# Kernel tuning notes

Hardware: AMD Instinct MI355X
Metric: run time of the kernel (lower is better)

## Reference

```python
import jax, jax.numpy as jnp
import numpy as np

E = 100000   # num entities
D = 300      # embedding dim
R = 1000     # num relations
T = 10000    # aligned pairs
K = 25       # negatives per pair
GAMMA = 1.0


def spmm(rows, cols, vals, x, n_rows):
    # sparse(COO) @ dense: out[r] = sum_{nnz: rows==r} vals * x[cols]
    return jax.ops.segment_sum(vals[:, None] * x[cols], rows, num_segments=n_rows)


def setup_inputs() -> dict:
    key = jax.random.key(0)
    ks = jax.random.split(key, 24)
    g = lambda i, s: jax.random.normal(ks[i], s, dtype=jnp.float32) * 0.05
    ri = lambda i, s, hi: jax.random.randint(ks[i], s, 0, hi, dtype=jnp.int32)
    ru = lambda i, s: jax.random.uniform(ks[i], s, dtype=jnp.float32)
    return {
        'word_embedding': jax.random.normal(ks[0], (E, D), dtype=jnp.float32),
        'kernel_gate': g(1, (D, D)),
        'bias_gate': jnp.zeros((D,), jnp.float32),
        'W1': g(2, (D, D)),
        'W2': g(3, (D, D)),
        'Dense': g(4, (3 * D, D)),
        'Bias': jnp.zeros((D,), jnp.float32),
        'hr_rows': ri(5, (300000,), R), 'hr_cols': ri(6, (300000,), E), 'hr_vals': ru(7, (300000,)),
        'tr_rows': ri(8, (300000,), R), 'tr_cols': ri(9, (300000,), E), 'tr_vals': ru(10, (300000,)),
        'er_rows': ri(11, (300000,), E), 'er_cols': ri(12, (300000,), 2 * R), 'er_vals': ru(13, (300000,)),
        'adj_rows': ri(14, (600000,), E), 'adj_cols': ri(15, (600000,), E), 'adj_vals': ru(16, (600000,)),
        'pos_left': ri(17, (T,), E), 'pos_right': ri(18, (T,), E),
        'neg_right': ri(19, (T, K), E), 'neg_left': ri(20, (T, K), E),
        'mask': jnp.ones((T, K), jnp.float32),
    }


def highway(layer1, layer2, kernel_gate, bias_gate):
    tg = jax.nn.sigmoid(layer1 @ kernel_gate + bias_gate)
    return tg * layer2 + (1.0 - tg) * layer1


def reference(word_embedding, kernel_gate, bias_gate, W1, W2, Dense, Bias,
              hr_rows, hr_cols, hr_vals, tr_rows, tr_cols, tr_vals,
              er_rows, er_cols, er_vals, adj_rows, adj_cols, adj_vals,
              pos_left, pos_right, neg_right, neg_left, mask):
    # L2-normalized frozen word embeddings
    emb = word_embedding / jnp.linalg.norm(word_embedding, axis=-1, keepdims=True)

    # Global relation aggregation (compute_r)
    L = spmm(hr_rows, hr_cols, hr_vals, emb, R)          # [R, D]
    Rm = spmm(tr_rows, tr_cols, tr_vals, emb, R)         # [R, D]
    r_fwd = jnp.concatenate([L, Rm], axis=-1)            # [R, 2D]
    r_emb = jnp.concatenate([r_fwd, -r_fwd], axis=0)     # [2R, 2D]
    nb = spmm(er_rows, er_cols, er_vals, r_emb, E)       # [E, 2D]
    h = jnp.concatenate([emb, nb], axis=-1)              # [E, 3D]
    h = emb + jax.nn.relu(h @ Dense + Bias)

    # Local relation aggregation: 2-layer highway GCN
    gcn1 = jax.nn.relu(spmm(adj_rows, adj_cols, adj_vals, h @ W1, E))
    hg1 = highway(h, gcn1, kernel_gate, bias_gate)
    gcn2 = jax.nn.relu(spmm(adj_rows, adj_cols, adj_vals, hg1 @ W2, E))
    node = highway(hg1, gcn2, kernel_gate, bias_gate)    # [E, D]

    # Hinge alignment loss
    l_x = node[pos_left]                                 # [T, D]
    r_x = node[pos_right]                                # [T, D]
    Dm = jnp.sum(jnp.abs(l_x - r_x), axis=1) + GAMMA     # [T]
    B1 = jnp.sum(jnp.abs(l_x[:, None, :] - node[neg_right]), axis=-1)  # [T, K]
    L1 = jax.nn.relu(Dm[:, None] - B1) * mask
    B2 = jnp.sum(jnp.abs(node[neg_left] - r_x[:, None, :]), axis=-1)   # [T, K]
    L2 = jax.nn.relu(Dm[:, None] - B2) * mask
    return (jnp.sum(L1) + jnp.sum(L2)) / 2.0
```

## Files before the change

### kernel.cpp

```cpp
#include <hip/hip_runtime.h>
#include <math.h>

#define E_N 100000
#define D_N 300
#define R_N 1000
#define T_N 10000
#define K_N 25
#define DP  320
#define BM  64
#define NT  1563

typedef __attribute__((ext_vector_type(8))) short bf16x8;
typedef __attribute__((ext_vector_type(4))) float f32x4;

__device__ __forceinline__ float bf2f(unsigned short h){
  union{ unsigned int u; float f; } c; c.u = ((unsigned int)h)<<16; return c.f;
}
__device__ __forceinline__ unsigned short f2bf(float f){
  union{ float f; unsigned int u; } c; c.f = f;
  unsigned int u = c.u + 0x7FFFu + ((c.u>>16)&1u);
  return (unsigned short)(u>>16);
}
__device__ __forceinline__ unsigned int pack2(float lo, float hi){
  return ((unsigned int)f2bf(hi)<<16) | f2bf(lo);
}

static constexpr size_t BUFB   = (size_t)100032*DP*2;
static constexpr size_t BUFU8  = (size_t)100032*DP;
static constexpr size_t OFF_B0    = 0;
static constexpr size_t OFF_B1    = BUFB;
static constexpr size_t OFF_B2    = 2*BUFB;
static constexpr size_t OFF_B3    = 3*BUFB;
static constexpr size_t OFF_RFWD  = OFF_B3 + BUFU8;
static constexpr size_t OFF_G     = OFF_RFWD + 1310720;
static constexpr size_t OFF_WTKG  = OFF_RFWD + 2400000;
static constexpr size_t OFF_WTW1  = OFF_WTKG + 204800;
static constexpr size_t OFF_WTW2  = OFF_WTW1 + 204800;
static constexpr size_t OFF_WTDN  = OFF_WTW2 + 204800;
static constexpr size_t OFF_WTDN2 = OFF_WTDN + 204800;
static constexpr size_t OFF_BIASP = OFF_WTDN2 + 409600;
static constexpr size_t OFF_BGP   = OFF_BIASP + 1280;
static constexpr size_t OFF_PTRHR = OFF_BGP + 1280;
static constexpr size_t OFF_PTRTR = OFF_PTRHR + 4096;
static constexpr size_t OFF_PTRER = OFF_PTRTR + 4096;
static constexpr size_t OFF_PTRADJ= OFF_PTRER + 400896;
static constexpr size_t OFF_CURHR = OFF_PTRADJ + 400896;
static constexpr size_t OFF_CURTR = OFF_CURHR + 4096;
static constexpr size_t OFF_CURER = OFF_CURTR + 4096;
static constexpr size_t OFF_CURADJ= OFF_CURER + 400896;
static constexpr size_t SZ_CURALL = 4096+4096+400896+400896;
static constexpr size_t OFF_SPHR  = OFF_CURADJ + 400896;
static constexpr size_t OFF_SPTR  = OFF_SPHR + 2400000;
static constexpr size_t OFF_SPER  = OFF_SPTR + 2400000;
static constexpr size_t OFF_SPAD  = OFF_SPER + 2400000;
static constexpr size_t OFF_PART  = OFF_SPAD + 4800000;
static constexpr size_t OFF_BSUM  = OFF_PART + 40000;

__device__ __forceinline__ size_t packIdx(int n, int k, int TK){
  return (size_t)(((n>>4)*TK + (k>>5))<<9) + (((k>>3)&3)<<7) + ((n&15)<<3) + (k&7);
}

__global__ void k_prep_sq(const float* kg, const float* w1, const float* w2,
                          unsigned short* wtKG, unsigned short* wtW1, unsigned short* wtW2){
  int n = blockIdx.x, which = blockIdx.y, k = threadIdx.x;
  const float* src = which==0 ? kg : (which==1 ? w1 : w2);
  unsigned short* dst = which==0 ? wtKG : (which==1 ? wtW1 : wtW2);
  float v = (n < D_N && k < D_N) ? src[k*D_N + n] : 0.f;
  dst[packIdx(n, k, 10)] = f2bf(v);
}

__global__ void k_prep_dense(const float* dn, unsigned short* wt, unsigned short* wt2){
  int n = blockIdx.x, t = threadIdx.x;
  {
    int k = t;
    float v = (n < D_N && k < D_N) ? dn[(size_t)k*D_N + n] : 0.f;
    wt[packIdx(n, k, 10)] = f2bf(v);
  }
  for(int k=t; k<640; k+=320){
    float v = (n < D_N && k < 600) ? dn[(size_t)(300+k)*D_N + n] : 0.f;
    wt2[packIdx(n, k, 20)] = f2bf(v);
  }
}

__global__ void k_prep_bias(const float* bias, const float* bg, float* biasP, float* bgP){
  int t = threadIdx.x;
  biasP[t] = (t < D_N) ? bias[t] : 0.f;
  bgP[t]   = (t < D_N) ? bg[t]   : 0.f;
}

__global__ __launch_bounds__(256) void k_normalize(const float* __restrict__ w,
                                                   unsigned short* __restrict__ embb){
  int wv = threadIdx.x >> 6, lane = threadIdx.x & 63;
  int e = blockIdx.x*4 + wv;
  const float4* row = (const float4*)(w + (size_t)e*D_N);
  float4 x0 = row[lane];
  float4 x1 = make_float4(0.f,0.f,0.f,0.f);
  if(lane < 11) x1 = row[64 + lane];
  float s = x0.x*x0.x + x0.y*x0.y + x0.z*x0.z + x0.w*x0.w
          + x1.x*x1.x + x1.y*x1.y + x1.z*x1.z + x1.w*x1.w;
  #pragma unroll
  for(int off=32; off; off>>=1) s += __shfl_xor(s, off);
  float rn = rsqrtf(s);
  unsigned short* orow = embb + (size_t)e*DP;
  uint2 o0; o0.x = pack2(x0.x*rn, x0.y*rn); o0.y = pack2(x0.z*rn, x0.w*rn);
  *(uint2*)(orow + lane*4) = o0;
  if(lane < 16){
    uint2 o1 = make_uint2(0u,0u);
    if(lane < 11){ o1.x = pack2(x1.x*rn, x1.y*rn); o1.y = pack2(x1.z*rn, x1.w*rn); }
    *(uint2*)(orow + 256 + lane*4) = o1;
  }
}

__global__ void k_count(const int* hr, const int* tr, const int* er, const int* ad,
                        int* cHR, int* cTR, int* cER, int* cAD){
  int i = (blockIdx.x*256 + threadIdx.x)*4;
  if(i < 300000){
    int4 r = *(const int4*)(hr + i);
    atomicAdd(&cHR[r.x],1); atomicAdd(&cHR[r.y],1);
    atomicAdd(&cHR[r.z],1); atomicAdd(&cHR[r.w],1);
  } else if(i < 600000){
    int4 r = *(const int4*)(tr + (i-300000));
    atomicAdd(&cTR[r.x],1); atomicAdd(&cTR[r.y],1);
    atomicAdd(&cTR[r.z],1); atomicAdd(&cTR[r.w],1);
  } else if(i < 900000){
    int4 r = *(const int4*)(er + (i-600000));
    atomicAdd(&cER[r.x],1); atomicAdd(&cER[r.y],1);
    atomicAdd(&cER[r.z],1); atomicAdd(&cER[r.w],1);
  } else if(i < 1500000){
    int4 r = *(const int4*)(ad + (i-900000));
    atomicAdd(&cAD[r.x],1); atomicAdd(&cAD[r.y],1);
    atomicAdd(&cAD[r.z],1); atomicAdd(&cAD[r.w],1);
  }
}

__global__ void k_scan_small(int* cHR, int* cTR, int* pHR, int* pTR){
  __shared__ int s[1024];
  int t = threadIdx.x;
  for(int w=0; w<2; w++){
    int* cnt = w ? cTR : cHR; int* ptr = w ? pTR : pHR;
    int c = (t < R_N) ? cnt[t] : 0;
    s[t] = c; __syncthreads();
    for(int off=1; off<1024; off<<=1){
      int v = (t>=off) ? s[t-off] : 0; __syncthreads();
      s[t] += v; __syncthreads();
    }
    int excl = s[t] - c;
    if(t < R_N){ ptr[t] = excl; cnt[t] = excl; }
    if(t == R_N-1) ptr[R_N] = s[t];
    __syncthreads();
  }
}

__global__ void k_scan_part(const int* cER, const int* cAD, int* pER, int* pAD, int* bsum){
  int which = blockIdx.y;
  const int* cnt = which ? cAD : cER;
  int* ptr = which ? pAD : pER;
  __shared__ int s[1024];
  int g = blockIdx.x, t = threadIdx.x, i = g*1024 + t;
  int c = (i < E_N) ? cnt[i] : 0;
  s[t] = c; __syncthreads();
  for(int off=1; off<1024; off<<=1){
    int v = (t>=off) ? s[t-off] : 0; __syncthreads();
    s[t] += v; __syncthreads();
  }
  if(i < E_N) ptr[i] = s[t] - c;
  if(t == 1023) bsum[which*128 + g] = s[1023];
}

__global__ void k_scan_mid(int* bsum, int* pER, int* pAD){
  __shared__ int s[128];
  int t = threadIdx.x;
  for(int w=0; w<2; w++){
    int v = (t < 98) ? bsum[w*128 + t] : 0;
    s[t] = v; __syncthreads();
    for(int off=1; off<128; off<<=1){
      int u = (t>=off) ? s[t-off] : 0; __syncthreads();
      s[t] += u; __syncthreads();
    }
    if(t < 98) bsum[w*128 + t] = s[t] - v;
    if(t == 97){ int* p = w ? pAD : pER; p[E_N] = s[97]; }
    __syncthreads();
  }
}

__global__ void k_scan_add(const int* bsum, int* pER, int* pAD, int* curER, int* curAD){
  int which = blockIdx.y;
  int* ptr = which ? pAD : pER;
  int* cur = which ? curAD : curER;
  int g = blockIdx.x, i = g*1024 + threadIdx.x;
  if(i < E_N){ int v = ptr[i] + bsum[which*128 + g]; ptr[i] = v; cur[i] = v; }
}

__global__ void k_scatter(const int* hr_r, const int* hr_c, const float* hr_v,
                          const int* tr_r, const int* tr_c, const float* tr_v,
                          const int* er_r, const int* er_c, const float* er_v,
                          const int* ad_r, const int* ad_c, const float* ad_v,
                          int* cHR, int* cTR, int* cER, int* cAD,
                          uint2* spHR, uint2* spTR, uint2* spER, uint2* spAD){
  int i = (blockIdx.x*256 + threadIdx.x)*4;
  const int* rp; const int* cp; const float* vp; int* cur; uint2* sp; int j;
  if(i < 300000){ rp=hr_r; cp=hr_c; vp=hr_v; cur=cHR; sp=spHR; j=i; }
  else if(i < 600000){ rp=tr_r; cp=tr_c; vp=tr_v; cur=cTR; sp=spTR; j=i-300000; }
  else if(i < 900000){ rp=er_r; cp=er_c; vp=er_v; cur=cER; sp=spER; j=i-600000; }
  else if(i < 1500000){ rp=ad_r; cp=ad_c; vp=ad_v; cur=cAD; sp=spAD; j=i-900000; }
  else return;
  int4 r = *(const int4*)(rp + j);
  int4 c = *(const int4*)(cp + j);
  float4 v = *(const float4*)(vp + j);
  int p0 = atomicAdd(&cur[r.x],1);
  int p1 = atomicAdd(&cur[r.y],1);
  int p2 = atomicAdd(&cur[r.z],1);
  int p3 = atomicAdd(&cur[r.w],1);
  sp[p0] = make_uint2((unsigned)c.x, __float_as_uint(v.x));
  sp[p1] = make_uint2((unsigned)c.y, __float_as_uint(v.y));
  sp[p2] = make_uint2((unsigned)c.z, __float_as_uint(v.z));
  sp[p3] = make_uint2((unsigned)c.w, __float_as_uint(v.w));
}

__global__ __launch_bounds__(256) void k_spmm_rel(
    const int* __restrict__ ptr, const uint2* __restrict__ sp,
    const unsigned short* __restrict__ embb, unsigned short* __restrict__ rfwdb, int off){
  int w = threadIdx.x >> 6, lane = threadIdx.x & 63;
  int r = blockIdx.x*2 + (w>>1);
  int half = w & 1;
  int elem = half*160 + 4*lane;
  bool act = (lane < 40) && (elem < 300);
  int b = ptr[r], e2 = ptr[r+1];
  float a0=0.f, a1=0.f, a2=0.f, a3=0.f;
  if(act){
    const unsigned short* base = embb + elem;
    int j = b;
    for(; j+4 <= e2; j += 4){
      uint2 q0=sp[j], q1=sp[j+1], q2=sp[j+2], q3=sp[j+3];
      int c0=(int)q0.x, c1=(int)q1.x, c2=(int)q2.x, c3=(int)q3.x;
      float v0=__uint_as_float(q0.y), v1=__uint_as_float(q1.y),
            v2=__uint_as_float(q2.y), v3=__uint_as_float(q3.y);
      uint2 x0 = *(const uint2*)(base + (size_t)c0*DP);
      uint2 x1 = *(const uint2*)(base + (size_t)c1*DP);
      uint2 x2 = *(const uint2*)(base + (size_t)c2*DP);
      uint2 x3 = *(const uint2*)(base + (size_t)c3*DP);
      a0 += v0*bf2f(x0.x&0xFFFF) + v1*bf2f(x1.x&0xFFFF) + v2*bf2f(x2.x&0xFFFF) + v3*bf2f(x3.x&0xFFFF);
      a1 += v0*bf2f(x0.x>>16)    + v1*bf2f(x1.x>>16)    + v2*bf2f(x2.x>>16)    + v3*bf2f(x3.x>>16);
      a2 += v0*bf2f(x0.y&0xFFFF) + v1*bf2f(x1.y&0xFFFF) + v2*bf2f(x2.y&0xFFFF) + v3*bf2f(x3.y&0xFFFF);
      a3 += v0*bf2f(x0.y>>16)    + v1*bf2f(x1.y>>16)    + v2*bf2f(x2.y>>16)    + v3*bf2f(x3.y>>16);
    }
    for(; j < e2; j++){
      uint2 q = sp[j];
      int c = (int)q.x; float v = __uint_as_float(q.y);
      uint2 x = *(const uint2*)(base + (size_t)c*DP);
      a0 += v*bf2f(x.x&0xFFFF); a1 += v*bf2f(x.x>>16);
      a2 += v*bf2f(x.y&0xFFFF); a3 += v*bf2f(x.y>>16);
    }
    uint2 o;
    o.x = pack2(a0, a1);
    o.y = pack2(a2, a3);
    *(uint2*)&rfwdb[(size_t)r*640 + off + elem] = o;
  }
}

__global__ __launch_bounds__(256) void k_gemm_G(const unsigned short* __restrict__ rfwdb,
    const unsigned short* __restrict__ Bt2, unsigned short* __restrict__ G){
  __shared__ unsigned short bufG[64][640];
  int tid = threadIdx.x;
  int wave = tid>>6, lane = tid&63, quad = lane>>4, l16 = lane&15;
  int m0 = blockIdx.x * 64;
  #pragma unroll
  for(int i=0; i<20; i++){
    int idx = tid + i*256;
    int row = idx/80, colc = idx%80;
    *(uint4*)&bufG[row][(colc ^ (row&7))*8] = *(const uint4*)(rfwdb + (size_t)(m0+row)*640 + colc*8);
  }
  __syncthreads();
  f32x4 acc[4][5];
  #pragma unroll
  for(int mf=0; mf<4; mf++)
    #pragma unroll
    for(int nf=0; nf<5; nf++) acc[mf][nf] = (f32x4){0.f,0.f,0.f,0.f};
  #pragma unroll 2
  for(int kk=0; kk<640; kk+=32){
    bf16x8 af[4], bfr[5];
    #pragma unroll
    for(int mf=0; mf<4; mf++)
      af[mf] = *(const bf16x8*)&bufG[mf*16 + l16][(((kk>>3)+quad) ^ (l16&7))*8];
    #pragma unroll
    for(int nf=0; nf<5; nf++)
      bfr[nf] = *(const bf16x8*)(Bt2 + ((size_t)(((wave*5+nf)*20 + (kk>>5))<<6) + lane)*8);
    #pragma unroll
    for(int mf=0; mf<4; mf++)
      #pragma unroll
      for(int nf=0; nf<5; nf++)
        acc[mf][nf] = __builtin_amdgcn_mfma_f32_16x16x32_bf16(af[mf], bfr[nf], acc[mf][nf], 0, 0, 0);
  }
  __syncthreads();
  unsigned short (*ob)[DP] = (unsigned short(*)[DP])bufG;
  #pragma unroll
  for(int mf=0; mf<4; mf++)
    #pragma unroll
    for(int nf=0; nf<5; nf++){
      int col = wave*80 + nf*16 + l16;
      #pragma unroll
      for(int i=0; i<4; i++){
        int rowl = mf*16 + quad*4 + i;
        ob[rowl][((col>>3) ^ (rowl&7))*8 + (col&7)] = f2bf(acc[mf][nf][i]);
      }
    }
  __syncthreads();
  #pragma unroll
  for(int i=0; i<10; i++){
    int idx = tid + i*256;
    int row = idx/40, colc = idx%40;
    *(uint4*)(G + (size_t)(m0+row)*DP + colc*8) = *(const uint4*)&ob[row][(colc ^ (row&7))*8];
  }
}

__global__ __launch_bounds__(256) void k_er_g(
    const int* __restrict__ ptr, const uint2* __restrict__ sp,
    const unsigned short* __restrict__ G, unsigned short* __restrict__ nb){
  int w = threadIdx.x >> 6, lane = threadIdx.x & 63;
  int e = blockIdx.x*4 + w;
  int b = ptr[e], en = ptr[e+1];
  if(lane < 40){
    float a0[8], a1[8];
    #pragma unroll
    for(int i=0;i<8;i++){ a0[i]=0.f; a1[i]=0.f; }
    const unsigned short* gb = G + lane*8;
    int j = b;
    for(; j+2 <= en; j += 2){
      uint2 q0=sp[j], q1=sp[j+1];
      int c0=(int)q0.x, c1=(int)q1.x;
      float v0=__uint_as_float(q0.y), v1=__uint_as_float(q1.y);
      int p0=c0, p1=c1;
      if(c0 >= R_N){ p0 = c0-R_N; v0 = -v0; }
      if(c1 >= R_N){ p1 = c1-R_N; v1 = -v1; }
      bf16x8 x0 = *(const bf16x8*)(gb + (size_t)p0*DP);
      bf16x8 x1 = *(const bf16x8*)(gb + (size_t)p1*DP);
      #pragma unroll
      for(int i=0;i<8;i++){ a0[i] += v0*bf2f((unsigned short)x0[i]);
                            a1[i] += v1*bf2f((unsigned short)x1[i]); }
    }
    if(j < en){
      uint2 q = sp[j];
      int c=(int)q.x; float v=__uint_as_float(q.y);
      int p=c; if(c >= R_N){ p = c-R_N; v = -v; }
      bf16x8 x = *(const bf16x8*)(gb + (size_t)p*DP);
      #pragma unroll
      for(int i=0;i<8;i++) a0[i] += v*bf2f((unsigned short)x[i]);
    }
    bf16x8 o;
    #pragma unroll
    for(int i=0;i<8;i++) o[i] = (short)f2bf(a0[i]+a1[i]);
    *(bf16x8*)&nb[(size_t)e*DP + lane*8] = o;
  }
}

__global__ __launch_bounds__(256) void k_spmm_hw(
    const int* __restrict__ ptr, const uint2* __restrict__ sp,
    const unsigned short* __restrict__ hw, const unsigned char* __restrict__ tg,
    const unsigned short* __restrict__ res, unsigned short* __restrict__ out){
  int w = threadIdx.x >> 6, lane = threadIdx.x & 63;
  int e = blockIdx.x*4 + w;
  int b = ptr[e], en = ptr[e+1];
  if(lane < 40){
    float a0[8], a1[8];
    #pragma unroll
    for(int i=0;i<8;i++){ a0[i]=0.f; a1[i]=0.f; }
    const unsigned short* base = hw + lane*8;
    int j = b;
    for(; j+2 <= en; j += 2){
      uint2 q0=sp[j], q1=sp[j+1];
      int c0=(int)q0.x, c1=(int)q1.x;
      float v0=__uint_as_float(q0.y), v1=__uint_as_float(q1.y);
      bf16x8 x0 = *(const bf16x8*)(base + (size_t)c0*DP);
      bf16x8 x1 = *(const bf16x8*)(base + (size_t)c1*DP);
      #pragma unroll
      for(int i=0;i<8;i++){ a0[i] += v0 * bf2f((unsigned short)x0[i]);
                            a1[i] += v1 * bf2f((unsigned short)x1[i]); }
    }
    if(j < en){
      uint2 q = sp[j];
      int c = (int)q.x; float v = __uint_as_float(q.y);
      bf16x8 x = *(const bf16x8*)(base + (size_t)c*DP);
      #pragma unroll
      for(int i=0;i<8;i++) a0[i] += v * bf2f((unsigned short)x[i]);
    }
    uint2 tu = *(const uint2*)(tg + (size_t)e*DP + lane*8);
    bf16x8 rv = *(const bf16x8*)(res + (size_t)e*DP + lane*8);
    bf16x8 o;
    #pragma unroll
    for(int i=0;i<8;i++){
      unsigned int word = (i<4) ? tu.x : tu.y;
      float g = (float)((word >> ((i&3)*8)) & 255u);
      g = (g + 0.5f) * 0.00390625f;
      float gcn = fmaxf(a0[i]+a1[i], 0.f);
      o[i] = (short)f2bf(g*gcn + (1.f-g)*bf2f(rv[i]));
    }
    *(bf16x8*)&out[(size_t)e*DP + lane*8] = o;
  }
}

__device__ __forceinline__ void stageA(unsigned short (*buf)[DP],
                                       const unsigned short* __restrict__ src, int tid){
  #pragma unroll
  for(int i=0; i<10; i++){
    int idx = tid + i*256;
    int row = idx/40, colc = idx%40;
    *(uint4*)&buf[row][(colc ^ (row&7))*8] = *(const uint4*)(src + (size_t)idx*8);
  }
}
__device__ __forceinline__ void storeT(unsigned short* dst,
                                       const unsigned short (*buf)[DP], int tid){
  #pragma unroll
  for(int i=0; i<10; i++){
    int idx = tid + i*256;
    int row = idx/40, colc = idx%40;
    *(uint4*)(dst + (size_t)idx*8) = *(const uint4*)&buf[row][(colc ^ (row&7))*8];
  }
}
__device__ __forceinline__ void storeT16(unsigned short* __restrict__ dst,
                                         const unsigned short (*buf)[DP], int tid){
  #pragma unroll
  for(int i=0; i<3; i++){
    int idx = tid + i*256;
    if(idx < 640){
      int row = idx/40, colc = idx%40;
      *(uint4*)(dst + (size_t)idx*8) = *(const uint4*)&buf[row][(colc ^ (row&7))*8];
    }
  }
}
__device__ __forceinline__ void kloop(f32x4 acc[4][5], const unsigned short (*As)[DP],
    const unsigned short* __restrict__ Bt, int TK, int tkb, int wave, int quad, int l16){
  int lane = (quad<<4) | l16;
  #pragma unroll 2
  for(int kk=0; kk<DP; kk+=32){
    bf16x8 af[4], bfr[5];
    #pragma unroll
    for(int mf=0; mf<4; mf++)
      af[mf] = *(const bf16x8*)&As[mf*16 + l16][(((kk>>3)+quad) ^ (l16&7))*8];
    #pragma unroll
    for(int nf=0; nf<5; nf++)
      bfr[nf] = *(const bf16x8*)(Bt + ((size_t)(((wave*5+nf)*TK + tkb + (kk>>5))<<6) + lane)*8);
    #pragma unroll
    for(int mf=0; mf<4; mf++)
      #pragma unroll
      for(int nf=0; nf<5; nf++)
        acc[mf][nf] = __builtin_amdgcn_mfma_f32_16x16x32_bf16(af[mf], bfr[nf], acc[mf][nf], 0, 0, 0);
  }
}

__global__ __launch_bounds__(256,3) void k_gemm_f(
    const unsigned short* __restrict__ Ain,
    const unsigned short* __restrict__ BtD,
    const unsigned short* nbG,
    const float* __restrict__ biasP,
    const unsigned short* __restrict__ BtW,
    const unsigned short* __restrict__ BtG,
    const float* __restrict__ bgP,
    unsigned short* hOut,
    unsigned short* __restrict__ hwOut,
    unsigned char*  __restrict__ tgOut,
    int dense){
  __shared__ unsigned short buf[BM][DP];
  __shared__ unsigned short scr[16][DP];
  int tid = threadIdx.x;
  int wave = tid>>6, lane = tid&63, quad = lane>>4, l16 = lane&15;
  int m0 = blockIdx.x * BM;

  stageA(buf, Ain + (size_t)m0*DP, tid);
  __syncthreads();

  if(dense){
    float breg[5];
    #pragma unroll
    for(int nf=0; nf<5; nf++) breg[nf] = biasP[wave*80 + nf*16 + l16];
    f32x4 acc[4][5];
    #pragma unroll
    for(int mf=0; mf<4; mf++)
      #pragma unroll
      for(int nf=0; nf<5; nf++) acc[mf][nf] = (f32x4){0.f,0.f,0.f,0.f};
    kloop(acc, buf, BtD, 10, 0, wave, quad, l16);
    const unsigned short* nbrow = nbG + (size_t)m0*DP;
    #pragma unroll
    for(int mf=0; mf<4; mf++){
      #pragma unroll
      for(int i=0; i<3; i++){
        int idx = tid + i*256;
        if(idx < 640){
          int row = idx/40, colc = idx%40;
          *(uint4*)&scr[row][(colc ^ (row&7))*8] =
              *(const uint4*)(nbrow + (size_t)(mf*16+row)*DP + colc*8);
        }
      }
      __syncthreads();
      #pragma unroll
      for(int nf=0; nf<5; nf++){
        int col = wave*80 + nf*16 + l16;
        #pragma unroll
        for(int i=0; i<4; i++){
          int rowl = mf*16 + quad*4 + i;
          int rloc = quad*4 + i;
          int a = ((col>>3) ^ (rowl&7))*8 + (col&7);
          float nbv  = bf2f(scr[rloc][((col>>3) ^ (rloc&7))*8 + (col&7)]);
          float resv = bf2f(buf[rowl][a]);
          buf[rowl][a] = f2bf(resv + fmaxf(acc[mf][nf][i] + breg[nf] + nbv, 0.f));
        }
      }
      __syncthreads();
    }
    storeT(hOut + (size_t)m0*DP, buf, tid);
  }

  {
    f32x4 acc[4][5];
    #pragma unroll
    for(int mf=0; mf<4; mf++)
      #pragma unroll
      for(int nf=0; nf<5; nf++) acc[mf][nf] = (f32x4){0.f,0.f,0.f,0.f};
    kloop(acc, buf, BtW, 10, 0, wave, quad, l16);
    #pragma unroll
    for(int mf=0; mf<4; mf++){
      #pragma unroll
      for(int nf=0; nf<5; nf++){
        int col = wave*80 + nf*16 + l16;
        #pragma unroll
        for(int i=0; i<4; i++){
          int rowl = quad*4 + i;
          scr[rowl][((col>>3) ^ (rowl&7))*8 + (col&7)] = f2bf(acc[mf][nf][i]);
        }
      }
      __syncthreads();
      storeT16(hwOut + (size_t)(m0 + mf*16)*DP, scr, tid);
      __syncthreads();
    }
  }

  {
    float greg[5];
    #pragma unroll
    for(int nf=0; nf<5; nf++) greg[nf] = bgP[wave*80 + nf*16 + l16];
    f32x4 acc[4][5];
    #pragma unroll
    for(int mf=0; mf<4; mf++)
      #pragma unroll
      for(int nf=0; nf<5; nf++) acc[mf][nf] = (f32x4){0.f,0.f,0.f,0.f};
    kloop(acc, buf, BtG, 10, 0, wave, quad, l16);
    unsigned char* bu = (unsigned char*)scr;
    #pragma unroll
    for(int c=0; c<2; c++){
      #pragma unroll
      for(int mh=0; mh<2; mh++){
        int mf = c*2 + mh;
        #pragma unroll
        for(int nf=0; nf<5; nf++){
          int col = wave*80 + nf*16 + l16;
          #pragma unroll
          for(int i=0; i<4; i++){
            int rowl = mh*16 + quad*4 + i;
            float tg = 1.f / (1.f + expf(-(acc[mf][nf][i] + greg[nf])));
            int u = (int)(tg * 256.f);
            u = u < 0 ? 0 : (u > 255 ? 255 : u);
            bu[rowl*DP + col] = (unsigned char)u;
          }
        }
      }
      __syncthreads();
      unsigned char* dst = tgOut + (size_t)(m0 + c*32)*DP;
      #pragma unroll
      for(int i=0; i<3; i++){
        int idx = tid + i*256;
        if(idx < 640) *(uint4*)(dst + (size_t)idx*16) = *(const uint4*)(bu + (size_t)idx*16);
      }
      __syncthreads();
    }
  }
}

__global__ __launch_bounds__(256) void k_loss(const unsigned short* __restrict__ node,
                       const int* __restrict__ pl, const int* __restrict__ pr,
                       const int* __restrict__ nr, const int* __restrict__ nl,
                       const float* __restrict__ mask,
                       float* __restrict__ part){
  int t = blockIdx.x;
  int w = threadIdx.x >> 6, lane = threadIdx.x & 63;
  __shared__ float wsum[4];
  bool act = lane < 40;
  size_t lb = (size_t)pl[t]*DP, rb = (size_t)pr[t]*DP;
  float lv[8], rv[8];
  #pragma unroll
  for(int i=0;i<8;i++){ lv[i]=0.f; rv[i]=0.f; }
  if(act){
    bf16x8 L = *(const bf16x8*)&node[lb + lane*8];
    bf16x8 R = *(const bf16x8*)&node[rb + lane*8];
    #pragma unroll
    for(int i=0;i<8;i++){ lv[i]=bf2f((unsigned short)L[i]); rv[i]=bf2f((unsigned short)R[i]); }
  }
  float s = 0.f;
  #pragma unroll
  for(int i=0;i<8;i++) s += fabsf(lv[i] - rv[i]);
  #pragma unroll
  for(int off=32; off; off>>=1) s += __shfl_xor(s, off);
  float dm = s + 1.0f;

  float local = 0.f;
  for(int k=w; k<K_N; k+=8){
    int k2 = k + 4;
    bool h2 = k2 < K_N;
    int kb = h2 ? k2 : k;
    float s1a=0.f, s2a=0.f, s1b=0.f, s2b=0.f;
    if(act){
      size_t nrb  = (size_t)nr[t*K_N+k ]*DP, nlb  = (size_t)nl[t*K_N+k ]*DP;
      size_t nrb2 = (size_t)nr[t*K_N+kb]*DP, nlb2 = (size_t)nl[t*K_N+kb]*DP;
      bf16x8 X1 = *(const bf16x8*)&node[nrb  + lane*8];
      bf16x8 Y1 = *(const bf16x8*)&node[nlb  + lane*8];
      bf16x8 X2 = *(const bf16x8*)&node[nrb2 + lane*8];
      bf16x8 Y2 = *(const bf16x8*)&node[nlb2 + lane*8];
      #pragma unroll
      for(int i=0;i<8;i++){
        s1a += fabsf(lv[i] - bf2f((unsigned short)X1[i]));
        s2a += fabsf(bf2f((unsigned short)Y1[i]) - rv[i]);
        s1b += fabsf(lv[i] - bf2f((unsigned short)X2[i]));
        s2b += fabsf(bf2f((unsigned short)Y2[i]) - rv[i]);
      }
    }
    #pragma unroll
    for(int off=32; off; off>>=1){
      s1a += __shfl_xor(s1a, off); s2a += __shfl_xor(s2a, off);
      s1b += __shfl_xor(s1b, off); s2b += __shfl_xor(s2b, off);
    }
    if(lane==0){
      local += (fmaxf(dm - s1a, 0.f) + fmaxf(dm - s2a, 0.f)) * mask[t*K_N+k];
      if(h2) local += (fmaxf(dm - s1b, 0.f) + fmaxf(dm - s2b, 0.f)) * mask[t*K_N+k2];
    }
  }
  if(lane==0) wsum[w] = local;
  __syncthreads();
  if(threadIdx.x==0) part[t] = wsum[0]+wsum[1]+wsum[2]+wsum[3];
}

__global__ void k_reduce(const float* part, float* out){
  __shared__ float s[256];
  int t = threadIdx.x;
  float a = 0.f;
  for(int i=t; i<T_N; i+=256) a += part[i];
  s[t] = a; __syncthreads();
  for(int off=128; off; off>>=1){ if(t<off) s[t]+=s[t+off]; __syncthreads(); }
  if(t==0) out[0] = s[0]*0.5f;
}

extern "C" void kernel_launch(void* const* d_in, const int* in_sizes, int n_in,
                              void* d_out, int out_size, void* d_ws, size_t ws_size,
                              hipStream_t stream){
  const float* Wemb = (const float*)d_in[0];
  const float* KG   = (const float*)d_in[1];
  const float* BG   = (const float*)d_in[2];
  const float* W1   = (const float*)d_in[3];
  const float* W2   = (const float*)d_in[4];
  const float* DN   = (const float*)d_in[5];
  const float* BI   = (const float*)d_in[6];
  const int* HRr = (const int*)d_in[7];  const int* HRc = (const int*)d_in[8];  const float* HRv = (const float*)d_in[9];
  const int* TRr = (const int*)d_in[10]; const int* TRc = (const int*)d_in[11]; const float* TRv = (const float*)d_in[12];
  const int* ERr = (const int*)d_in[13]; const int* ERc = (const int*)d_in[14]; const float* ERv = (const float*)d_in[15];
  const int* ADr = (const int*)d_in[16]; const int* ADc = (const int*)d_in[17]; const float* ADv = (const float*)d_in[18];
  const int* PL = (const int*)d_in[19]; const int* PR = (const int*)d_in[20];
  const int* NR = (const int*)d_in[21]; const int* NL = (const int*)d_in[22];
  const float* MASK = (const float*)d_in[23];
  char* ws = (char*)d_ws;

  unsigned short* B0 = (unsigned short*)(ws + OFF_B0);
  unsigned short* B1 = (unsigned short*)(ws + OFF_B1);
  unsigned short* B2 = (unsigned short*)(ws + OFF_B2);
  unsigned char*  B3 = (unsigned char*)(ws + OFF_B3);
  unsigned short* rfwdb = (unsigned short*)(ws + OFF_RFWD);
  unsigned short* Gb    = (unsigned short*)(ws + OFF_G);
  unsigned short* wtKG = (unsigned short*)(ws + OFF_WTKG);
  unsigned short* wtW1 = (unsigned short*)(ws + OFF_WTW1);
  unsigned short* wtW2 = (unsigned short*)(ws + OFF_WTW2);
  unsigned short* wtDN = (unsigned short*)(ws + OFF_WTDN);
  unsigned short* wtDN2= (unsigned short*)(ws + OFF_WTDN2);
  float* biasP = (float*)(ws + OFF_BIASP);
  float* bgP   = (float*)(ws + OFF_BGP);
  int* pHR = (int*)(ws + OFF_PTRHR); int* pTR = (int*)(ws + OFF_PTRTR);
  int* pER = (int*)(ws + OFF_PTRER); int* pAD = (int*)(ws + OFF_PTRADJ);
  int* cHR = (int*)(ws + OFF_CURHR); int* cTR = (int*)(ws + OFF_CURTR);
  int* cER = (int*)(ws + OFF_CURER); int* cAD = (int*)(ws + OFF_CURADJ);
  uint2* spHR = (uint2*)(ws + OFF_SPHR);
  uint2* spTR = (uint2*)(ws + OFF_SPTR);
  uint2* spER = (uint2*)(ws + OFF_SPER);
  uint2* spAD = (uint2*)(ws + OFF_SPAD);
  float* part = (float*)(ws + OFF_PART);
  int* bsum   = (int*)(ws + OFF_BSUM);

  (void)hipMemsetAsync(ws + OFF_CURHR, 0, SZ_CURALL, stream);
  (void)hipMemsetAsync(ws + OFF_RFWD, 0, 1310720, stream);

  k_prep_sq<<<dim3(320,3), 320, 0, stream>>>(KG, W1, W2, wtKG, wtW1, wtW2);
  k_prep_dense<<<320, 320, 0, stream>>>(DN, wtDN, wtDN2);
  k_prep_bias<<<1, 320, 0, stream>>>(BI, BG, biasP, bgP);
  k_normalize<<<E_N/4, 256, 0, stream>>>(Wemb, B0);

  k_count<<<1465, 256, 0, stream>>>(HRr, TRr, ERr, ADr, cHR, cTR, cER, cAD);
  k_scan_small<<<1, 1024, 0, stream>>>(cHR, cTR, pHR, pTR);
  k_scan_part<<<dim3(98,2), 1024, 0, stream>>>(cER, cAD, pER, pAD, bsum);
  k_scan_mid<<<1, 128, 0, stream>>>(bsum, pER, pAD);
  k_scan_add<<<dim3(98,2), 1024, 0, stream>>>(bsum, pER, pAD, cER, cAD);
  k_scatter<<<1465, 256, 0, stream>>>(HRr,HRc,HRv, TRr,TRc,TRv, ERr,ERc,ERv, ADr,ADc,ADv,
                                      cHR,cTR,cER,cAD, spHR, spTR, spER, spAD);

  k_spmm_rel<<<R_N/2, 256, 0, stream>>>(pHR, spHR, B0, rfwdb, 0);
  k_spmm_rel<<<R_N/2, 256, 0, stream>>>(pTR, spTR, B0, rfwdb, 300);

  k_gemm_G<<<16, 256, 0, stream>>>(rfwdb, wtDN2, Gb);
  k_er_g<<<E_N/4, 256, 0, stream>>>(pER, spER, Gb, B1);

  k_gemm_f<<<NT, 256, 0, stream>>>(B0, wtDN, B1, biasP,
                                   wtW1, wtKG, bgP, B1, B2, B3, 1);
  k_spmm_hw<<<E_N/4, 256, 0, stream>>>(pAD, spAD, B2, B3, B1, B0);
  k_gemm_f<<<NT, 256, 0, stream>>>(B0, nullptr, nullptr, nullptr,
                                   wtW2, wtKG, bgP, nullptr, B2, B3, 0);
  k_spmm_hw<<<E_N/4, 256, 0, stream>>>(pAD, spAD, B2, B3, B0, B1);

  k_loss<<<T_N, 256, 0, stream>>>(B1, PL, PR, NR, NL, MASK, part);
  k_reduce<<<1, 256, 0, stream>>>(part, (float*)d_out);
}
```

Measured before the change: 1.140 ms.

## Replace global-atomic COO-to-CSR scatter with two-pass bucketed staging scatter

The COO-to-CSR conversion now bins each nonzero into a coarse row-bucket staging area during the counting pass, with the local row index packed into the high bits of the column. A new per-bucket kernel then scatters the entries into their final CSR slots using shared-memory cursors instead of global atomics on per-row cursors. The intent is to cut random global atomic traffic and scattered writes in the CSR build. In exchange it adds a staging buffer that aliases B2 and fixed per-bucket capacities, which could overflow with skewed row distributions. It also relies on column indices fitting in 17 bits.

```diff
diff --git a/kernel.cpp b/kernel.cpp
--- a/kernel.cpp
+++ b/kernel.cpp
@@ -9,6 +9,12 @@
 #define DP  320
 #define BM  64
 #define NT  1563
+
+#define NB_E   782
+#define NB_R   125
+#define CAP_AD 256
+#define CAP_ER 128
+#define CAP_RT 512
 
 typedef __attribute__((ext_vector_type(8))) short bf16x8;
 typedef __attribute__((ext_vector_type(4))) float f32x4;
@@ -55,6 +61,15 @@
 static constexpr size_t OFF_SPAD  = OFF_SPER + 2400000;
 static constexpr size_t OFF_PART  = OFF_SPAD + 4800000;
 static constexpr size_t OFF_BSUM  = OFF_PART + 40000;
+static constexpr size_t OFF_BCAD  = OFF_BSUM + 4096;
+static constexpr size_t OFF_BCER  = OFF_BCAD + 25600;
+static constexpr size_t OFF_BCHR  = OFF_BCER + 25600;
+static constexpr size_t OFF_BCTR  = OFF_BCHR + 4096;
+static constexpr size_t SZ_BCALL  = 25600+25600+4096+4096;
+static constexpr size_t OFF_STAD  = OFF_B2;
+static constexpr size_t OFF_STER  = OFF_STAD + (size_t)NB_E*8*CAP_AD*8;
+static constexpr size_t OFF_STHR  = OFF_STER + (size_t)NB_E*8*CAP_ER*8;
+static constexpr size_t OFF_STTR  = OFF_STHR + (size_t)NB_R*8*CAP_RT*8;
 
 __device__ __forceinline__ size_t packIdx(int n, int k, int TK){
   return (size_t)(((n>>4)*TK + (k>>5))<<9) + (((k>>3)&3)<<7) + ((n&15)<<3) + (k&7);
@@ -111,25 +126,71 @@
   }
 }
 
-__global__ void k_count(const int* hr, const int* tr, const int* er, const int* ad,
-                        int* cHR, int* cTR, int* cER, int* cAD){
-  int i = (blockIdx.x*256 + threadIdx.x)*4;
-  if(i < 300000){
-    int4 r = *(const int4*)(hr + i);
-    atomicAdd(&cHR[r.x],1); atomicAdd(&cHR[r.y],1);
-    atomicAdd(&cHR[r.z],1); atomicAdd(&cHR[r.w],1);
-  } else if(i < 600000){
-    int4 r = *(const int4*)(tr + (i-300000));
-    atomicAdd(&cTR[r.x],1); atomicAdd(&cTR[r.y],1);
-    atomicAdd(&cTR[r.z],1); atomicAdd(&cTR[r.w],1);
-  } else if(i < 900000){
-    int4 r = *(const int4*)(er + (i-600000));
-    atomicAdd(&cER[r.x],1); atomicAdd(&cER[r.y],1);
-    atomicAdd(&cER[r.z],1); atomicAdd(&cER[r.w],1);
-  } else if(i < 1500000){
-    int4 r = *(const int4*)(ad + (i-900000));
-    atomicAdd(&cAD[r.x],1); atomicAdd(&cAD[r.y],1);
-    atomicAdd(&cAD[r.z],1); atomicAdd(&cAD[r.w],1);
+__global__ __launch_bounds__(256) void k_phaseA(
+    const int* hr_r, const int* hr_c, const float* hr_v,
+    const int* tr_r, const int* tr_c, const float* tr_v,
+    const int* er_r, const int* er_c, const float* er_v,
+    const int* ad_r, const int* ad_c, const float* ad_v,
+    int* cHR, int* cTR, int* cER, int* cAD,
+    int* bcHR, int* bcTR, int* bcER, int* bcAD,
+    uint2* stHR, uint2* stTR, uint2* stER, uint2* stAD){
+  int g8 = blockIdx.x & 7;
+  int i = (blockIdx.x*256 + threadIdx.x)*2;
+  const int* rp; const int* cp; const float* vp; int* cnt; int* bc; uint2* st;
+  int j, shift, cap;
+  if(i < 300000){ rp=hr_r; cp=hr_c; vp=hr_v; cnt=cHR; bc=bcHR; st=stHR; j=i;        shift=3; cap=CAP_RT; }
+  else if(i < 600000){ rp=tr_r; cp=tr_c; vp=tr_v; cnt=cTR; bc=bcTR; st=stTR; j=i-300000; shift=3; cap=CAP_RT; }
+  else if(i < 900000){ rp=er_r; cp=er_c; vp=er_v; cnt=cER; bc=bcER; st=stER; j=i-600000; shift=7; cap=CAP_ER; }
+  else if(i < 1500000){ rp=ad_r; cp=ad_c; vp=ad_v; cnt=cAD; bc=bcAD; st=stAD; j=i-900000; shift=7; cap=CAP_AD; }
+  else return;
+  int2 r = *(const int2*)(rp + j);
+  int2 c = *(const int2*)(cp + j);
+  float2 v = *(const float2*)(vp + j);
+  atomicAdd(&cnt[r.x], 1);
+  atomicAdd(&cnt[r.y], 1);
+  int m = (1<<shift) - 1;
+  int sb0 = ((r.x>>shift)<<3) + g8;
+  int sb1 = ((r.y>>shift)<<3) + g8;
+  int p0 = atomicAdd(&bc[sb0], 1);
+  int p1 = atomicAdd(&bc[sb1], 1);
+  st[(size_t)sb0*cap + p0] = make_uint2(((unsigned)(r.x&m)<<17)|(unsigned)c.x, __float_as_uint(v.x));
+  st[(size_t)sb1*cap + p1] = make_uint2(((unsigned)(r.y&m)<<17)|(unsigned)c.y, __float_as_uint(v.y));
+}
+
+__global__ __launch_bounds__(256) void k_bscatter(
+    const uint2* __restrict__ stAD, const uint2* __restrict__ stER,
+    const uint2* __restrict__ stHR, const uint2* __restrict__ stTR,
+    const int* __restrict__ bcAD, const int* __restrict__ bcER,
+    const int* __restrict__ bcHR, const int* __restrict__ bcTR,
+    const int* __restrict__ pAD, const int* __restrict__ pER,
+    const int* __restrict__ pHR, const int* __restrict__ pTR,
+    uint2* spAD, uint2* spER, uint2* spHR, uint2* spTR){
+  __shared__ int cur[128];
+  int b = blockIdx.x, tid = threadIdx.x;
+  const uint2* st; const int* bc; const int* ptr; uint2* sp;
+  int base, nrows, cap, maxrow;
+  if(b < NB_E){            st=stAD; bc=bcAD; ptr=pAD; sp=spAD; base=b;           nrows=128; cap=CAP_AD; maxrow=E_N; }
+  else if(b < 2*NB_E){     st=stER; bc=bcER; ptr=pER; sp=spER; base=b-NB_E;      nrows=128; cap=CAP_ER; maxrow=E_N; }
+  else if(b < 2*NB_E+NB_R){st=stHR; bc=bcHR; ptr=pHR; sp=spHR; base=b-2*NB_E;    nrows=8;   cap=CAP_RT; maxrow=R_N; }
+  else {                   st=stTR; bc=bcTR; ptr=pTR; sp=spTR; base=b-2*NB_E-NB_R; nrows=8; cap=CAP_RT; maxrow=R_N; }
+  int r0 = base*nrows;
+  if(tid < nrows){
+    int row = r0 + tid;
+    cur[tid] = (row < maxrow) ? ptr[row] : 0;
+  }
+  __syncthreads();
+  #pragma unroll 1
+  for(int s=0; s<8; s++){
+    int sb = base*8 + s;
+    int cnt = bc[sb];
+    const uint2* src = st + (size_t)sb*cap;
+    for(int j=tid; j<cnt; j+=256){
+      uint2 q = src[j];
+      int rl = (int)(q.x >> 17);
+      unsigned col = q.x & 0x1FFFFu;
+      int p = atomicAdd(&cur[rl], 1);
+      sp[p] = make_uint2(col, q.y);
+    }
   }
 }
 
@@ -144,8 +205,7 @@
       int v = (t>=off) ? s[t-off] : 0; __syncthreads();
       s[t] += v; __syncthreads();
     }
-    int excl = s[t] - c;
-    if(t < R_N){ ptr[t] = excl; cnt[t] = excl; }
+    if(t < R_N) ptr[t] = s[t] - c;
     if(t == R_N-1) ptr[R_N] = s[t];
     __syncthreads();
   }
@@ -183,38 +243,11 @@
   }
 }
 
-__global__ void k_scan_add(const int* bsum, int* pER, int* pAD, int* curER, int* curAD){
+__global__ void k_scan_add(const int* bsum, int* pER, int* pAD){
   int which = blockIdx.y;
   int* ptr = which ? pAD : pER;
-  int* cur = which ? curAD : curER;
   int g = blockIdx.x, i = g*1024 + threadIdx.x;
-  if(i < E_N){ int v = ptr[i] + bsum[which*128 + g]; ptr[i] = v; cur[i] = v; }
-}
-
-__global__ void k_scatter(const int* hr_r, const int* hr_c, const float* hr_v,
-                          const int* tr_r, const int* tr_c, const float* tr_v,
-                          const int* er_r, const int* er_c, const float* er_v,
-                          const int* ad_r, const int* ad_c, const float* ad_v,
-                          int* cHR, int* cTR, int* cER, int* cAD,
-                          uint2* spHR, uint2* spTR, uint2* spER, uint2* spAD){
-  int i = (blockIdx.x*256 + threadIdx.x)*4;
-  const int* rp; const int* cp; const float* vp; int* cur; uint2* sp; int j;
-  if(i < 300000){ rp=hr_r; cp=hr_c; vp=hr_v; cur=cHR; sp=spHR; j=i; }
-  else if(i < 600000){ rp=tr_r; cp=tr_c; vp=tr_v; cur=cTR; sp=spTR; j=i-300000; }
-  else if(i < 900000){ rp=er_r; cp=er_c; vp=er_v; cur=cER; sp=spER; j=i-600000; }
-  else if(i < 1500000){ rp=ad_r; cp=ad_c; vp=ad_v; cur=cAD; sp=spAD; j=i-900000; }
-  else return;
-  int4 r = *(const int4*)(rp + j);
-  int4 c = *(const int4*)(cp + j);
-  float4 v = *(const float4*)(vp + j);
-  int p0 = atomicAdd(&cur[r.x],1);
-  int p1 = atomicAdd(&cur[r.y],1);
-  int p2 = atomicAdd(&cur[r.z],1);
-  int p3 = atomicAdd(&cur[r.w],1);
-  sp[p0] = make_uint2((unsigned)c.x, __float_as_uint(v.x));
-  sp[p1] = make_uint2((unsigned)c.y, __float_as_uint(v.y));
-  sp[p2] = make_uint2((unsigned)c.z, __float_as_uint(v.z));
-  sp[p3] = make_uint2((unsigned)c.w, __float_as_uint(v.w));
+  if(i < E_N) ptr[i] += bsum[which*128 + g];
 }
 
 __global__ __launch_bounds__(256) void k_spmm_rel(
@@ -688,8 +721,13 @@
   uint2* spAD = (uint2*)(ws + OFF_SPAD);
   float* part = (float*)(ws + OFF_PART);
   int* bsum   = (int*)(ws + OFF_BSUM);
+  int* bcAD = (int*)(ws + OFF_BCAD); int* bcER = (int*)(ws + OFF_BCER);
+  int* bcHR = (int*)(ws + OFF_BCHR); int* bcTR = (int*)(ws + OFF_BCTR);
+  uint2* stAD = (uint2*)(ws + OFF_STAD); uint2* stER = (uint2*)(ws + OFF_STER);
+  uint2* stHR = (uint2*)(ws + OFF_STHR); uint2* stTR = (uint2*)(ws + OFF_STTR);
 
   (void)hipMemsetAsync(ws + OFF_CURHR, 0, SZ_CURALL, stream);
+  (void)hipMemsetAsync(ws + OFF_BCAD, 0, SZ_BCALL, stream);
   (void)hipMemsetAsync(ws + OFF_RFWD, 0, 1310720, stream);
 
   k_prep_sq<<<dim3(320,3), 320, 0, stream>>>(KG, W1, W2, wtKG, wtW1, wtW2);
@@ -697,13 +735,17 @@
   k_prep_bias<<<1, 320, 0, stream>>>(BI, BG, biasP, bgP);
   k_normalize<<<E_N/4, 256, 0, stream>>>(Wemb, B0);
 
-  k_count<<<1465, 256, 0, stream>>>(HRr, TRr, ERr, ADr, cHR, cTR, cER, cAD);
+  k_phaseA<<<2930, 256, 0, stream>>>(HRr,HRc,HRv, TRr,TRc,TRv, ERr,ERc,ERv, ADr,ADc,ADv,
+                                     cHR,cTR,cER,cAD, bcHR,bcTR,bcER,bcAD,
+                                     stHR,stTR,stER,stAD);
   k_scan_small<<<1, 1024, 0, stream>>>(cHR, cTR, pHR, pTR);
   k_scan_part<<<dim3(98,2), 1024, 0, stream>>>(cER, cAD, pER, pAD, bsum);
   k_scan_mid<<<1, 128, 0, stream>>>(bsum, pER, pAD);
-  k_scan_add<<<dim3(98,2), 1024, 0, stream>>>(bsum, pER, pAD, cER, cAD);
-  k_scatter<<<1465, 256, 0, stream>>>(HRr,HRc,HRv, TRr,TRc,TRv, ERr,ERc,ERv, ADr,ADc,ADv,
-                                      cHR,cTR,cER,cAD, spHR, spTR, spER, spAD);
+  k_scan_add<<<dim3(98,2), 1024, 0, stream>>>(bsum, pER, pAD);
+  k_bscatter<<<2*NB_E + 2*NB_R, 256, 0, stream>>>(stAD, stER, stHR, stTR,
+                                                  bcAD, bcER, bcHR, bcTR,
+                                                  pAD, pER, pHR, pTR,
+                                                  spAD, spER, spHR, spTR);
 
   k_spmm_rel<<<R_N/2, 256, 0, stream>>>(pHR, spHR, B0, rfwdb, 0);
   k_spmm_rel<<<R_N/2, 256, 0, stream>>>(pTR, spTR, B0, rfwdb, 300);
```

New measurement: 1.095 ms. -3.9%, faster.
